# Optimization experiments

Measured on AMD Instinct MI355X. Metric: run time of the kernel, lower is better.

Reference implementation:

```python
import jax, jax.numpy as jnp
import numpy as np

DIM = 768
B, N = 8, 2048


def setup_inputs() -> dict:
    key = jax.random.key(0)
    k = jax.random.split(key, 8)
    s = 1.0 / np.sqrt(DIM)
    return {
        "x": jax.random.normal(k[0], (B, N, DIM), jnp.float32),
        "x2": jax.random.normal(k[1], (B, N, DIM), jnp.float32),
        "x3": jax.random.normal(k[2], (B, N, DIM), jnp.float32),
        "W1": jax.random.uniform(k[3], (DIM, DIM), jnp.float32, -s, s),
        "b1": jax.random.uniform(k[4], (DIM,), jnp.float32, -s, s),
        "W2": jax.random.uniform(k[5], (DIM, DIM), jnp.float32, -s, s),
        "b2": jax.random.uniform(k[6], (DIM,), jnp.float32, -s, s),
        "w": jnp.ones((1,), jnp.float32),
    }


def _cross_attention(x, x2, W, b):
    # key = softmax(x2.transpose(1,2), dim=1) -> softmax over feature axis, then [B, D, N]
    key = jnp.swapaxes(jax.nn.softmax(x2, axis=-1), 1, 2)  # [B, D, N]
    query = jax.nn.softmax(x2, axis=1)                      # [B, N, D], softmax over tokens
    context = jnp.einsum('bnd,bdm->bnm', x, key)            # [B, N, N]
    atten = jnp.einsum('bnm,bmd->bnd', context, query)      # [B, N, D]
    return atten @ W.T + b


def reference(x, x2, x3, W1, b1, W2, b2, w):
    a1 = _cross_attention(x, x2, W1, b1)
    a2 = _cross_attention(x, x3, W2, b2)
    f = jax.nn.sigmoid(w)  # scalar gate, broadcast
    atten = a1 * f + a2 * f
    return atten + x
```

## Files before the change

kernel.cpp:

```cpp
#include <hip/hip_runtime.h>

#define DIMD 768
#define NTOK 2048
#define NB   8

typedef __attribute__((ext_vector_type(8))) short bfrag8;
typedef __attribute__((ext_vector_type(4))) float accf4;

__device__ __forceinline__ unsigned short f2bf(float f) {
  unsigned u = __float_as_uint(f);
  return (unsigned short)((u + 0x7fffu + ((u >> 16) & 1u)) >> 16);
}

__device__ __forceinline__ void glds16(const void* g, void* l) {
  __builtin_amdgcn_global_load_lds(
      (const __attribute__((address_space(1))) void*)g,
      (__attribute__((address_space(3))) void*)l, 16, 0, 0);
}


__device__ __forceinline__ void packw_body(int blk, const float* __restrict__ W1,
                                           const float* __restrict__ W2,
                                           unsigned short* __restrict__ Wcat) {
  int gid = blk * 256 + threadIdx.x;
  int r = gid / 192, c4 = (gid % 192) * 4;
  float4 a = *(const float4*)(W1 + (size_t)r * DIMD + c4);
  float4 b = *(const float4*)(W2 + (size_t)r * DIMD + c4);
  union { unsigned short us[4]; uint2 u2; } ra, rb;
  ra.us[0] = f2bf(a.x); ra.us[1] = f2bf(a.y); ra.us[2] = f2bf(a.z); ra.us[3] = f2bf(a.w);
  rb.us[0] = f2bf(b.x); rb.us[1] = f2bf(b.y); rb.us[2] = f2bf(b.z); rb.us[3] = f2bf(b.w);
  *(uint2*)(Wcat + (size_t)r * 1536 + c4) = ra.u2;
  *(uint2*)(Wcat + (size_t)r * 1536 + 768 + c4) = rb.u2;
}

__device__ __forceinline__ void packx_body(int blk, const float* __restrict__ x,
                                           unsigned short* __restrict__ xb) {
  size_t gid = (size_t)blk * 256 + threadIdx.x;
  const float4* x4 = (const float4*)x;
  float4 v0 = x4[gid * 2], v1 = x4[gid * 2 + 1];
  union { unsigned short us[8]; uint4 u4; } r;
  r.us[0] = f2bf(v0.x); r.us[1] = f2bf(v0.y); r.us[2] = f2bf(v0.z); r.us[3] = f2bf(v0.w);
  r.us[4] = f2bf(v1.x); r.us[5] = f2bf(v1.y); r.us[6] = f2bf(v1.z); r.us[7] = f2bf(v1.w);
  ((uint4*)xb)[gid] = r.u4;
}

template <int TMD, int TND, int EPI>
__device__ __forceinline__ void gemm_body(
    unsigned short* As, unsigned short* Bs, int bid,
    const unsigned short* __restrict__ A, const unsigned short* __restrict__ B,
    void* __restrict__ Cout, int K, int lda, int ldb, int ldc, int ntx,
    long long sA, long long sB, long long sC,
    const float* __restrict__ wg, const float* __restrict__ b1v,
    const float* __restrict__ b2v, const float* __restrict__ xres) {
  constexpr int TM = 64 * TMD, TN = 64 * TND;
  __shared__ float csi[64 * TND];
  const int t = threadIdx.x, w = t >> 6, lane = t & 63;
  const int bz = bid & 7;
  const int r = bid >> 3;
  const int by = r / ntx, bx = r - by * ntx;
  const int m0 = by * TM, n0 = bx * TN;
  const unsigned short* Ab = A + (size_t)bz * sA;
  const unsigned short* Bb = B + (size_t)bz * sB;
  const int srow = lane >> 3;
  const int scol = (lane & 7) * 8;

  if (EPI == 2) {
    for (int c = t; c < TN; c += 256) {
      const float* cp = b1v + (size_t)bz * 32 * DIMD + n0 + c;
      float s = 0.f;
#pragma unroll
      for (int p = 0; p < 32; ++p) s += cp[(size_t)p * DIMD];
      csi[c] = 1.0f / s;
    }
  }

  accf4 zero = {0.f, 0.f, 0.f, 0.f};
  accf4 acc[2 * TMD][2 * TND];
#pragma unroll
  for (int i = 0; i < 2 * TMD; ++i)
#pragma unroll
    for (int j = 0; j < 2 * TND; ++j) acc[i][j] = zero;

  const int wm = (w & 1) * (32 * TMD), wn = (w >> 1) * (32 * TND);
  const int lm = lane & 15, qd = lane >> 4;

  for (int k0 = 0; k0 < K; k0 += 64) {
    __syncthreads();
#pragma unroll
    for (int l = 0; l < 2 * TND; ++l) {
      int chunk = l * 4 + w;
      int row = chunk * 8 + srow;
      glds16(Bb + (size_t)(n0 + row) * ldb + k0 + scol,
             (char*)Bs + chunk * 1024 + lane * 16);
    }
#pragma unroll
    for (int l = 0; l < 2 * TMD; ++l) {
      int chunk = l * 4 + w;
      int row = chunk * 8 + srow;
      glds16(Ab + (size_t)(m0 + row) * lda + k0 + scol,
             (char*)As + chunk * 1024 + lane * 16);
    }
    __syncthreads();
#pragma unroll
    for (int kc = 0; kc < 2; ++kc) {
      bfrag8 av[2 * TMD], bv[2 * TND];
#pragma unroll
      for (int i = 0; i < 2 * TMD; ++i)
        av[i] = *(const bfrag8*)(As + (wm + i * 16 + lm) * 64 + kc * 32 + qd * 8);
#pragma unroll
      for (int j = 0; j < 2 * TND; ++j)
        bv[j] = *(const bfrag8*)(Bs + (wn + j * 16 + lm) * 64 + kc * 32 + qd * 8);
#pragma unroll
      for (int i = 0; i < 2 * TMD; ++i)
#pragma unroll
        for (int j = 0; j < 2 * TND; ++j)
          acc[i][j] = __builtin_amdgcn_mfma_f32_16x16x32_bf16(av[i], bv[j], acc[i][j], 0, 0, 0);
    }
  }

  if (EPI == 0) {
    unsigned short* Cb = (unsigned short*)Cout + (size_t)bz * sC;
#pragma unroll
    for (int i = 0; i < 2 * TMD; ++i)
#pragma unroll
      for (int j = 0; j < 2 * TND; ++j) {
        int col = n0 + wn + j * 16 + lm;
#pragma unroll
        for (int rr = 0; rr < 4; ++rr) {
          int row = m0 + wm + i * 16 + qd * 4 + rr;
          Cb[(size_t)row * ldc + col] = f2bf(acc[i][j][rr]);
        }
      }
  } else if (EPI == 1) {
    float gate = 1.f / (1.f + __expf(-wg[0]));
    float* Co = (float*)Cout + (size_t)bz * sC;
    const float* Xr = xres + (size_t)bz * sC;
#pragma unroll
    for (int j = 0; j < 2 * TND; ++j) {
      int col = n0 + wn + j * 16 + lm;
      float gb = gate * (b1v[col] + b2v[col]);
#pragma unroll
      for (int i = 0; i < 2 * TMD; ++i)
#pragma unroll
        for (int rr = 0; rr < 4; ++rr) {
          int row = m0 + wm + i * 16 + qd * 4 + rr;
          size_t idx = (size_t)row * ldc + col;
          Co[idx] = gate * acc[i][j][rr] + gb + Xr[idx];
        }
    }
  } else {
    unsigned short* Cb = (unsigned short*)Cout + (size_t)bz * sC;
#pragma unroll
    for (int j = 0; j < 2 * TND; ++j) {
      int lc = wn + j * 16 + lm;
      int col = n0 + lc;
      float ci = csi[lc];
#pragma unroll
      for (int i = 0; i < 2 * TMD; ++i)
#pragma unroll
        for (int rr = 0; rr < 4; ++rr) {
          int row = m0 + wm + i * 16 + qd * 4 + rr;
          Cb[(size_t)row * ldc + col] = f2bf(acc[i][j][rr] * ci);
        }
    }
  }
}


__global__ __launch_bounds__(256) void prep_kernel(const float* __restrict__ W1,
                                                   const float* __restrict__ W2,
                                                   unsigned short* __restrict__ Wcat,
                                                   const float* __restrict__ x2,
                                                   const float* __restrict__ x3,
                                                   float* __restrict__ rs1,
                                                   float* __restrict__ rs2) {
  int blk = blockIdx.x;
  if (blk < 576) { packw_body(blk, W1, W2, Wcat); return; }
  int rblk = blk - 576;
  const float* src = (rblk < 4096) ? x2 : x3;
  float* dst = (rblk < 4096) ? rs1 : rs2;
  int q = rblk & 4095;
  int w = threadIdx.x >> 6, lane = threadIdx.x & 63;
  int row = q * 4 + w;
  const float* r = src + (size_t)row * DIMD;
  float s = 0.f;
#pragma unroll
  for (int j = 0; j < 12; ++j) s += __expf(r[lane + j * 64]);
#pragma unroll
  for (int off = 32; off; off >>= 1) s += __shfl_xor(s, off, 64);
  if (lane == 0) dst[row] = 1.0f / s;
}

__global__ __launch_bounds__(256) void sm_kq(
    const float* __restrict__ xA, const float* __restrict__ rsA,
    unsigned short* __restrict__ KtA, unsigned short* __restrict__ QtA,
    float* __restrict__ cspA,
    const float* __restrict__ xB, const float* __restrict__ rsB,
    unsigned short* __restrict__ KtB, unsigned short* __restrict__ QtB,
    float* __restrict__ cspB) {
  int z = blockIdx.z;
  const float* xin; const float* rsv; unsigned short* Kt; unsigned short* Qt;
  float* csp; int b;
  if (z < 8) { xin = xA; rsv = rsA; Kt = KtA; Qt = QtA; csp = cspA; b = z; }
  else       { xin = xB; rsv = rsB; Kt = KtB; Qt = QtB; csp = cspB; b = z - 8; }
  const int n0 = blockIdx.x * 64, dc = blockIdx.y;
  const int t = threadIdx.x;
  __shared__ float rowsi[64];
  __shared__ __align__(16) unsigned short etile[128 * 72];
  if (t < 64) rowsi[t] = rsv[(size_t)b * NTOK + n0 + t];
  const float* xbase = xin + ((size_t)b * NTOK + n0) * DIMD + dc * 128;
  const int tok = t >> 2, g0 = t & 3;
#pragma unroll
  for (int p = 0; p < 8; ++p) {
    int dg = g0 + p * 4;
    float4 v = *(const float4*)(xbase + (size_t)tok * DIMD + dg * 4);
    int dl = dg * 4;
    etile[(dl + 0) * 72 + tok] = f2bf(__expf(v.x));
    etile[(dl + 1) * 72 + tok] = f2bf(__expf(v.y));
    etile[(dl + 2) * 72 + tok] = f2bf(__expf(v.z));
    etile[(dl + 3) * 72 + tok] = f2bf(__expf(v.w));
  }
  __syncthreads();
#pragma unroll
  for (int q = 0; q < 4; ++q) {
    int dl = (t >> 3) + q * 32;
    int g = t & 7;
    uint4 e8 = *(const uint4*)(etile + dl * 72 + g * 8);
    float ef[8];
    ef[0] = __uint_as_float(e8.x << 16); ef[1] = __uint_as_float(e8.x & 0xffff0000u);
    ef[2] = __uint_as_float(e8.y << 16); ef[3] = __uint_as_float(e8.y & 0xffff0000u);
    ef[4] = __uint_as_float(e8.z << 16); ef[5] = __uint_as_float(e8.z & 0xffff0000u);
    ef[6] = __uint_as_float(e8.w << 16); ef[7] = __uint_as_float(e8.w & 0xffff0000u);
    float4 r0 = *(const float4*)&rowsi[g * 8];
    float4 r1 = *(const float4*)&rowsi[g * 8 + 4];
    union { unsigned short us[8]; uint4 u4; } ko;
    ko.us[0] = f2bf(ef[0] * r0.x); ko.us[1] = f2bf(ef[1] * r0.y);
    ko.us[2] = f2bf(ef[2] * r0.z); ko.us[3] = f2bf(ef[3] * r0.w);
    ko.us[4] = f2bf(ef[4] * r1.x); ko.us[5] = f2bf(ef[5] * r1.y);
    ko.us[6] = f2bf(ef[6] * r1.z); ko.us[7] = f2bf(ef[7] * r1.w);
    size_t orow = ((size_t)b * DIMD + dc * 128 + dl) * NTOK + n0 + g * 8;
    *(uint4*)(Kt + orow) = ko.u4;
    *(uint4*)(Qt + orow) = e8;
    float s = ((ef[0] + ef[1]) + (ef[2] + ef[3])) + ((ef[4] + ef[5]) + (ef[6] + ef[7]));
    s += __shfl_xor(s, 1, 64);
    s += __shfl_xor(s, 2, 64);
    s += __shfl_xor(s, 4, 64);
    if (g == 0) csp[((size_t)b * 32 + blockIdx.x) * DIMD + dc * 128 + dl] = s;
  }
}

template <int TMD, int TND, int EPI>
__global__ __launch_bounds__(256) void mfma_bt(
    const unsigned short* __restrict__ A, const unsigned short* __restrict__ B,
    void* __restrict__ Cout, int K, int lda, int ldb, int ldc, int ntx,
    long long sA, long long sB, long long sC,
    const float* __restrict__ wg, const float* __restrict__ b1v,
    const float* __restrict__ b2v, const float* __restrict__ xres) {
  __shared__ __align__(16) unsigned short As[64 * TMD * 64];
  __shared__ __align__(16) unsigned short Bs[64 * TND * 64];
  gemm_body<TMD, TND, EPI>(As, Bs, blockIdx.x, A, B, Cout, K, lda, ldb, ldc, ntx,
                           sA, sB, sC, wg, b1v, b2v, xres);
}

__global__ __launch_bounds__(256) void sgemm_s(
    const unsigned short* __restrict__ KtA, const unsigned short* __restrict__ QtA,
    const float* __restrict__ cspA,
    const unsigned short* __restrict__ KtB, const unsigned short* __restrict__ QtB,
    const float* __restrict__ cspB,
    unsigned short* __restrict__ Ca, unsigned short* __restrict__ Cb) {
  __shared__ __align__(16) unsigned short As[128 * 64];
  __shared__ __align__(16) unsigned short Bs[128 * 64];
  bool second = blockIdx.x >= 288;
  const unsigned short* A = second ? KtB : KtA;
  const unsigned short* B = second ? QtB : QtA;
  const float* csp = second ? cspB : cspA;
  unsigned short* C = second ? Cb : Ca;
  int blk = second ? (blockIdx.x - 288) : blockIdx.x;
  gemm_body<2, 2, 2>(As, Bs, blk, A, B, C, NTOK, NTOK, NTOK, 1536, 6,
                     768LL * NTOK, 768LL * NTOK, 768LL * 1536,
                     nullptr, csp, nullptr, nullptr);
}

__global__ __launch_bounds__(256) void s2_packx_kernel(
    const unsigned short* __restrict__ Wcat, const unsigned short* __restrict__ Scat,
    unsigned short* __restrict__ Bt, const float* __restrict__ x,
    unsigned short* __restrict__ xb) {
  __shared__ __align__(16) unsigned short As[128 * 64];
  __shared__ __align__(16) unsigned short Bs[128 * 64];
  int blk = blockIdx.x;
  if (blk < 288) {
    gemm_body<2, 2, 0>(As, Bs, blk, Wcat, Scat, Bt, 1536, 1536, 1536, 768, 6,
                       0LL, 768LL * 1536, 768LL * 768,
                       nullptr, nullptr, nullptr, nullptr);
  } else {
    packx_body(blk - 288, x, xb);
  }
}

extern "C" void kernel_launch(void* const* d_in, const int* in_sizes, int n_in,
                              void* d_out, int out_size, void* d_ws, size_t ws_size,
                              hipStream_t stream) {
  const float* x  = (const float*)d_in[0];
  const float* x2 = (const float*)d_in[1];
  const float* x3 = (const float*)d_in[2];
  const float* W1 = (const float*)d_in[3];
  const float* b1 = (const float*)d_in[4];
  const float* W2 = (const float*)d_in[5];
  const float* b2 = (const float*)d_in[6];
  const float* w  = (const float*)d_in[7];
  float* out = (float*)d_out;
  char* ws = (char*)d_ws;

  dim3 blk(256);
  const bool merged = ws_size >= 123600896ull;

  if (merged) {
    unsigned short* Kt1  = (unsigned short*)(ws + 0);
    unsigned short* Qt1  = (unsigned short*)(ws + 25165824);
    unsigned short* Kt2  = (unsigned short*)(ws + 50331648);
    unsigned short* Qt2  = (unsigned short*)(ws + 75497472);
    unsigned short* Scat = (unsigned short*)(ws + 100663296);
    unsigned short* Wcat = (unsigned short*)(ws + 119537664);
    float* csp1 = (float*)(ws + 121896960);
    float* csp2 = (float*)(ws + 122683392);
    float* rs1  = (float*)(ws + 123469824);
    float* rs2  = (float*)(ws + 123535360);
    unsigned short* Bt = (unsigned short*)(ws + 0);
    unsigned short* xb = (unsigned short*)(ws + 9437184);

    prep_kernel<<<8768, blk, 0, stream>>>(W1, W2, Wcat, x2, x3, rs1, rs2);
    sm_kq<<<dim3(32, 6, 16), blk, 0, stream>>>(x2, rs1, Kt1, Qt1, csp1,
                                               x3, rs2, Kt2, Qt2, csp2);
    sgemm_s<<<576, blk, 0, stream>>>(Kt1, Qt1, csp1, Kt2, Qt2, csp2, Scat, Scat + 768);
    s2_packx_kernel<<<6432, blk, 0, stream>>>(Wcat, Scat, Bt, x, xb);
    mfma_bt<2, 2, 1><<<768, blk, 0, stream>>>(xb, Bt, out, DIMD, DIMD, DIMD, DIMD, 6,
                                              (long long)NTOK * DIMD, 768LL * 768,
                                              (long long)NTOK * DIMD, w, b1, b2, x);
  } else {
    unsigned short* Kt   = (unsigned short*)(ws + 0);
    unsigned short* Qt   = (unsigned short*)(ws + 25165824);
    unsigned short* Scat = (unsigned short*)(ws + 50331648);
    unsigned short* Bt   = (unsigned short*)(ws + 69206016);
    float* csp1 = (float*)(ws + 69206016);
    float* csp2 = (float*)(ws + 69992448);
    float* rs1  = (float*)(ws + 70778880);
    float* rs2  = (float*)(ws + 70844416);
    unsigned short* xb   = (unsigned short*)(ws + 78643200);
    unsigned short* Wcat = (unsigned short*)(ws + 103809024);

    prep_kernel<<<8768, blk, 0, stream>>>(W1, W2, Wcat, x2, x3, rs1, rs2);
    sm_kq<<<dim3(32, 6, 8), blk, 0, stream>>>(x2, rs1, Kt, Qt, csp1,
                                              x2, rs1, Kt, Qt, csp1);
    sgemm_s<<<288, blk, 0, stream>>>(Kt, Qt, csp1, Kt, Qt, csp1, Scat, Scat);
    sm_kq<<<dim3(32, 6, 8), blk, 0, stream>>>(x3, rs2, Kt, Qt, csp2,
                                              x3, rs2, Kt, Qt, csp2);
    sgemm_s<<<288, blk, 0, stream>>>(Kt, Qt, csp2, Kt, Qt, csp2, Scat + 768, Scat + 768);
    s2_packx_kernel<<<6432, blk, 0, stream>>>(Wcat, Scat, Bt, x, xb);
    mfma_bt<2, 2, 1><<<768, blk, 0, stream>>>(xb, Bt, out, DIMD, DIMD, DIMD, DIMD, 6,
                                              (long long)NTOK * DIMD, 768LL * 768,
                                              (long long)NTOK * DIMD, w, b1, b2, x);
  }
}
```

Before: 380.3 us.

## Double-buffer LDS tiles in GEMM main loop to overlap loads with MFMA

```diff
diff --git a/kernel.cpp b/kernel.cpp
--- a/kernel.cpp
+++ b/kernel.cpp
@@ -53,6 +53,7 @@
     const float* __restrict__ wg, const float* __restrict__ b1v,
     const float* __restrict__ b2v, const float* __restrict__ xres) {
   constexpr int TM = 64 * TMD, TN = 64 * TND;
+  constexpr int ASZ = TM * 64, BSZ = TN * 64;
   __shared__ float csi[64 * TND];
   const int t = threadIdx.x, w = t >> 6, lane = t & 63;
   const int bz = bid & 7;
@@ -64,6 +65,27 @@
   const int srow = lane >> 3;
   const int scol = (lane & 7) * 8;
 
+  auto stage = [&](int buf, int k0) {
+    unsigned short* Ad = As + buf * ASZ;
+    unsigned short* Bd = Bs + buf * BSZ;
+#pragma unroll
+    for (int l = 0; l < 2 * TND; ++l) {
+      int chunk = l * 4 + w;
+      int row = chunk * 8 + srow;
+      glds16(Bb + (size_t)(n0 + row) * ldb + k0 + scol,
+             (char*)Bd + chunk * 1024 + lane * 16);
+    }
+#pragma unroll
+    for (int l = 0; l < 2 * TMD; ++l) {
+      int chunk = l * 4 + w;
+      int row = chunk * 8 + srow;
+      glds16(Ab + (size_t)(m0 + row) * lda + k0 + scol,
+             (char*)Ad + chunk * 1024 + lane * 16);
+    }
+  };
+
+  stage(0, 0);
+
   if (EPI == 2) {
     for (int c = t; c < TN; c += 256) {
       const float* cp = b1v + (size_t)bz * 32 * DIMD + n0 + c;
@@ -84,38 +106,36 @@
   const int wm = (w & 1) * (32 * TMD), wn = (w >> 1) * (32 * TND);
   const int lm = lane & 15, qd = lane >> 4;
 
-  for (int k0 = 0; k0 < K; k0 += 64) {
-    __syncthreads();
-#pragma unroll
-    for (int l = 0; l < 2 * TND; ++l) {
-      int chunk = l * 4 + w;
-      int row = chunk * 8 + srow;
-      glds16(Bb + (size_t)(n0 + row) * ldb + k0 + scol,
-             (char*)Bs + chunk * 1024 + lane * 16);
-    }
-#pragma unroll
-    for (int l = 0; l < 2 * TMD; ++l) {
-      int chunk = l * 4 + w;
-      int row = chunk * 8 + srow;
-      glds16(Ab + (size_t)(m0 + row) * lda + k0 + scol,
-             (char*)As + chunk * 1024 + lane * 16);
-    }
-    __syncthreads();
+  __syncthreads();
+
+  const int nt = K / 64;
+  int cur = 0;
+#pragma unroll 2
+  for (int tt = 0; tt < nt; ++tt) {
+    if (tt + 1 < nt) stage(cur ^ 1, (tt + 1) * 64);
+    const unsigned short* Ar = As + cur * ASZ;
+    const unsigned short* Br = Bs + cur * BSZ;
 #pragma unroll
     for (int kc = 0; kc < 2; ++kc) {
       bfrag8 av[2 * TMD], bv[2 * TND];
 #pragma unroll
       for (int i = 0; i < 2 * TMD; ++i)
-        av[i] = *(const bfrag8*)(As + (wm + i * 16 + lm) * 64 + kc * 32 + qd * 8);
+        av[i] = *(const bfrag8*)(Ar + (wm + i * 16 + lm) * 64 + kc * 32 + qd * 8);
 #pragma unroll
       for (int j = 0; j < 2 * TND; ++j)
-        bv[j] = *(const bfrag8*)(Bs + (wn + j * 16 + lm) * 64 + kc * 32 + qd * 8);
+        bv[j] = *(const bfrag8*)(Br + (wn + j * 16 + lm) * 64 + kc * 32 + qd * 8);
+      __builtin_amdgcn_s_setprio(1);
 #pragma unroll
       for (int i = 0; i < 2 * TMD; ++i)
 #pragma unroll
         for (int j = 0; j < 2 * TND; ++j)
           acc[i][j] = __builtin_amdgcn_mfma_f32_16x16x32_bf16(av[i], bv[j], acc[i][j], 0, 0, 0);
-    }
+      __builtin_amdgcn_s_setprio(0);
+    }
+    if (tt + 1 < nt) {
+      asm volatile("s_waitcnt vmcnt(0)\n\ts_barrier" ::: "memory");
+    }
+    cur ^= 1;
   }
 
   if (EPI == 0) {
@@ -256,8 +276,8 @@
     long long sA, long long sB, long long sC,
     const float* __restrict__ wg, const float* __restrict__ b1v,
     const float* __restrict__ b2v, const float* __restrict__ xres) {
-  __shared__ __align__(16) unsigned short As[64 * TMD * 64];
-  __shared__ __align__(16) unsigned short Bs[64 * TND * 64];
+  __shared__ __align__(16) unsigned short As[2 * 64 * TMD * 64];
+  __shared__ __align__(16) unsigned short Bs[2 * 64 * TND * 64];
   gemm_body<TMD, TND, EPI>(As, Bs, blockIdx.x, A, B, Cout, K, lda, ldb, ldc, ntx,
                            sA, sB, sC, wg, b1v, b2v, xres);
 }
@@ -268,8 +288,8 @@
     const unsigned short* __restrict__ KtB, const unsigned short* __restrict__ QtB,
     const float* __restrict__ cspB,
     unsigned short* __restrict__ Ca, unsigned short* __restrict__ Cb) {
-  __shared__ __align__(16) unsigned short As[128 * 64];
-  __shared__ __align__(16) unsigned short Bs[128 * 64];
+  __shared__ __align__(16) unsigned short As[2 * 128 * 64];
+  __shared__ __align__(16) unsigned short Bs[2 * 128 * 64];
   bool second = blockIdx.x >= 288;
   const unsigned short* A = second ? KtB : KtA;
   const unsigned short* B = second ? QtB : QtA;
@@ -285,8 +305,8 @@
     const unsigned short* __restrict__ Wcat, const unsigned short* __restrict__ Scat,
     unsigned short* __restrict__ Bt, const float* __restrict__ x,
     unsigned short* __restrict__ xb) {
-  __shared__ __align__(16) unsigned short As[128 * 64];
-  __shared__ __align__(16) unsigned short Bs[128 * 64];
+  __shared__ __align__(16) unsigned short As[2 * 128 * 64];
+  __shared__ __align__(16) unsigned short Bs[2 * 128 * 64];
   int blk = blockIdx.x;
   if (blk < 288) {
     gemm_body<2, 2, 0>(As, Bs, blk, Wcat, Scat, Bt, 1536, 1536, 1536, 768, 6,
```

New measurement: 356.2 us. 1.07x faster.
